# Kernel tuning notes

Measured on AMD Instinct MI355X. Metric: run time of the kernel, lower is better.

The kernel has to match this reference:

```python
import jax, jax.numpy as jnp
import numpy as np

NUM_SEGMENTS = 64
HIDDEN = 1024
RANK = 16
N = 8192


def _xavier(key, shape):
    fan_in, fan_out = shape[-2], shape[-1]
    limit = (6.0 / (fan_in + fan_out)) ** 0.5
    return jax.random.uniform(key, shape, jnp.float32, -limit, limit)


def setup_inputs() -> dict:
    key = jax.random.key(0)
    k1, k2, k3, k4 = jax.random.split(key, 4)
    return {
        "math_hidden_states": jax.random.normal(k1, (N, HIDDEN), jnp.float32),
        "segment_ids": jax.random.randint(k2, (N,), 0, NUM_SEGMENTS, jnp.int64),
        "A_matrices": _xavier(k3, (NUM_SEGMENTS, HIDDEN, RANK)),
        "B_matrices": _xavier(k4, (NUM_SEGMENTS, RANK, HIDDEN)),
        "bias": jnp.zeros((NUM_SEGMENTS, HIDDEN), jnp.float32),
    }


def reference(math_hidden_states, segment_ids, A_matrices, B_matrices, bias):
    # gather per-token low-rank factors: A [N,H,R], B [N,R,H]
    gathered_A = A_matrices[segment_ids]
    gathered_B = B_matrices[segment_ids]
    # intermediate = B @ x  -> [N, R]
    intermediate = jnp.einsum('nrh,nh->nr', gathered_B, math_hidden_states)
    # transformed = A @ intermediate -> [N, H]
    transformed = jnp.einsum('nhr,nr->nh', gathered_A, intermediate)
    return transformed + bias[segment_ids]
```

## Files before the change

### kernel.cpp

```cpp
#include <hip/hip_runtime.h>

#define HID 1024
#define RANK 16
#define NSEG 64
#define NCHUNK 16
#define NXCD 8

__global__ __launch_bounds__(256) void lora_v5(
    const float* __restrict__ x,
    const int*   __restrict__ seg,
    const float* __restrict__ A,
    const float* __restrict__ B,
    const float* __restrict__ bias,
    float*       __restrict__ out,
    int N)
{
    const int work = (blockIdx.x & (NXCD - 1)) * ((NSEG * NCHUNK) / NXCD)
                   + (blockIdx.x >> 3);
    const int s = work >> 4;
    const int c = work & (NCHUNK - 1);
    const int tid  = threadIdx.x;
    const int lane = tid & 63;
    const int wave = tid >> 6;

    __shared__ int   list[512];
    __shared__ int   cnt;
    __shared__ float red[4][16][68];
    __shared__ float inter_lds[2][4][RANK];

    if (tid == 0) cnt = 0;

    const float4* A4 = (const float4*)(A + (size_t)s * HID * RANK);
    float4 av[4][4];
    #pragma unroll
    for (int jh = 0; jh < 4; ++jh)
        #pragma unroll
        for (int q = 0; q < 4; ++q)
            av[jh][q] = A4[(size_t)(tid * 4 + jh) * (RANK / 4) + q];
    const float4 bia = ((const float4*)(bias + (size_t)s * HID))[tid];

    __syncthreads();

    const int chunkN = (N + NCHUNK - 1) / NCHUNK;
    const int i0 = c * chunkN;
    const int i1 = min(N, i0 + chunkN);
    for (int i = i0 + tid; i < i1; i += 256)
        if (seg[i] == s) list[atomicAdd(&cnt, 1)] = i;
    __syncthreads();
    const int m = cnt;
    if (m == 0) return;

    const float4* B4 = (const float4*)(B + (size_t)s * RANK * HID);
    const int v = lane & 15;
    const int q = lane >> 4;

    for (int t = 0; t < m; t += 4) {
        const int nt = min(4, m - t);
        int n[4];
        #pragma unroll
        for (int j = 0; j < 4; ++j)
            n[j] = list[t + (j < nt ? j : nt - 1)];

        float4 xv[4][4];
        #pragma unroll
        for (int j = 0; j < 4; ++j) {
            const float4* xr = (const float4*)(x + (size_t)n[j] * HID);
            #pragma unroll
            for (int k = 0; k < 4; ++k) xv[j][k] = xr[k * 64 + lane];
        }

        float acc[4][4];
        #pragma unroll
        for (int rr = 0; rr < 4; ++rr)
            #pragma unroll
            for (int j = 0; j < 4; ++j) acc[rr][j] = 0.f;

        #pragma unroll
        for (int rr = 0; rr < 4; ++rr) {
            const float4* Br = B4 + (size_t)(wave * 4 + rr) * (HID / 4);
            #pragma unroll
            for (int k = 0; k < 4; ++k) {
                float4 b = Br[k * 64 + lane];
                #pragma unroll
                for (int j = 0; j < 4; ++j)
                    acc[rr][j] += b.x * xv[j][k].x + b.y * xv[j][k].y
                                + b.z * xv[j][k].z + b.w * xv[j][k].w;
            }
        }

        #pragma unroll
        for (int rr = 0; rr < 4; ++rr)
            #pragma unroll
            for (int j = 0; j < 4; ++j)
                red[wave][rr * 4 + j][lane] = acc[rr][j];

        const float4* rp = (const float4*)&red[wave][v][q * 16];
        float4 r0 = rp[0], r1 = rp[1], r2 = rp[2], r3 = rp[3];
        float sum = ((r0.x + r0.y) + (r0.z + r0.w))
                  + ((r1.x + r1.y) + (r1.z + r1.w))
                  + ((r2.x + r2.y) + (r2.z + r2.w))
                  + ((r3.x + r3.y) + (r3.z + r3.w));
        sum += __shfl_xor(sum, 16, 64);
        sum += __shfl_xor(sum, 32, 64);

        const int buf = (t >> 2) & 1;
        if (lane < 16)
            inter_lds[buf][v & 3][wave * 4 + (v >> 2)] = sum;
        __syncthreads();

        #pragma unroll
        for (int j = 0; j < 4; ++j) {
            const float4* I4 = (const float4*)inter_lds[buf][j];
            float4 iv[4];
            #pragma unroll
            for (int qq = 0; qq < 4; ++qq) iv[qq] = I4[qq];
            float4 o = bia;
            float* op = (float*)&o;
            #pragma unroll
            for (int jh = 0; jh < 4; ++jh) {
                float a = 0.f;
                #pragma unroll
                for (int qq = 0; qq < 4; ++qq)
                    a += av[jh][qq].x * iv[qq].x + av[jh][qq].y * iv[qq].y
                       + av[jh][qq].z * iv[qq].z + av[jh][qq].w * iv[qq].w;
                op[jh] += a;
            }
            if (j < nt)
                ((float4*)(out + (size_t)n[j] * HID))[tid] = o;
        }
    }
}

extern "C" void kernel_launch(void* const* d_in, const int* in_sizes, int n_in,
                              void* d_out, int out_size, void* d_ws, size_t ws_size,
                              hipStream_t stream) {
    const float* x    = (const float*)d_in[0];
    const int*   seg  = (const int*)d_in[1];
    const float* A    = (const float*)d_in[2];
    const float* B    = (const float*)d_in[3];
    const float* bias = (const float*)d_in[4];
    float* out = (float*)d_out;

    const int n_tokens = in_sizes[1];

    lora_v5<<<NSEG * NCHUNK, 256, 0, stream>>>(x, seg, A, B, bias, out, n_tokens);
}
```

Measured before the change: 114.7 us.

## Replace per-chunk segment scanning with histogram-sort and one-tile-per-block apply

Adds a single-block histogram kernel and an atomic scatter kernel that bucket token indices by segment into a padded sorted list. The apply kernel then processes exactly one tile of four tokens per block. This removes the per-block scan of a whole chunk of segment ids (each id was read by all 64 segment blocks) and the serial inner loop over tokens. In exchange it adds two extra kernel launches, including a serial single-block histogram. It also reloads A and bias for every tile instead of reusing them across tokens.

```diff
diff --git a/kernel.cpp b/kernel.cpp
--- a/kernel.cpp
+++ b/kernel.cpp
@@ -3,32 +3,80 @@
 #define HID 1024
 #define RANK 16
 #define NSEG 64
-#define NCHUNK 16
 #define NXCD 8
 
-__global__ __launch_bounds__(256) void lora_v5(
+
+__global__ __launch_bounds__(1024) void k1_hist(
+    const int* __restrict__ seg, int N,
+    int* __restrict__ base_c, int* __restrict__ cursor,
+    int* __restrict__ sorted, int slots)
+{
+    __shared__ int hist[NSEG];
+    __shared__ int pbase[NSEG];
+    __shared__ int paddedTotal;
+    const int tid = threadIdx.x;
+    if (tid < NSEG) hist[tid] = 0;
+    __syncthreads();
+    for (int i = tid; i < N; i += 1024) atomicAdd(&hist[seg[i]], 1);
+    __syncthreads();
+    if (tid == 0) {
+        int run = 0;
+        for (int s = 0; s < NSEG; ++s) { pbase[s] = run; run += (hist[s] + 3) & ~3; }
+        paddedTotal = run;
+    }
+    __syncthreads();
+    if (tid < NSEG) {
+        base_c[tid] = pbase[tid];
+        cursor[tid] = 0;
+        const int c0 = hist[tid], c1 = (hist[tid] + 3) & ~3;
+        for (int k = c0; k < c1; ++k) sorted[pbase[tid] + k] = -1;
+    }
+    for (int i = paddedTotal + tid; i < slots; i += 1024) sorted[i] = -1;
+}
+
+__global__ __launch_bounds__(256) void k2_scatter(
+    const int* __restrict__ seg, int N,
+    const int* __restrict__ base_c, int* __restrict__ cursor,
+    int* __restrict__ sorted)
+{
+    const int i = blockIdx.x * 256 + threadIdx.x;
+    if (i < N) {
+        const int s = seg[i];
+        const int pos = atomicAdd(&cursor[s], 1);
+        sorted[base_c[s] + pos] = (s << 14) | i;
+    }
+}
+
+__global__ __launch_bounds__(256) void lora_apply(
     const float* __restrict__ x,
-    const int*   __restrict__ seg,
+    const int*   __restrict__ sorted,
     const float* __restrict__ A,
     const float* __restrict__ B,
     const float* __restrict__ bias,
     float*       __restrict__ out,
-    int N)
+    int tilesPerXcd)
 {
-    const int work = (blockIdx.x & (NXCD - 1)) * ((NSEG * NCHUNK) / NXCD)
-                   + (blockIdx.x >> 3);
-    const int s = work >> 4;
-    const int c = work & (NCHUNK - 1);
+    const int work = (blockIdx.x & (NXCD - 1)) * tilesPerXcd + (blockIdx.x >> 3);
     const int tid  = threadIdx.x;
     const int lane = tid & 63;
     const int wave = tid >> 6;
 
-    __shared__ int   list[512];
-    __shared__ int   cnt;
     __shared__ float red[4][16][68];
-    __shared__ float inter_lds[2][4][RANK];
+    __shared__ float inter_lds[4][RANK];
 
-    if (tid == 0) cnt = 0;
+    int e[4];
+    #pragma unroll
+    for (int j = 0; j < 4; ++j) e[j] = sorted[work * 4 + j];
+    if (e[0] < 0) return;
+    const int s = e[0] >> 14;
+
+    int  n[4];
+    bool valid[4];
+    #pragma unroll
+    for (int j = 0; j < 4; ++j) {
+        valid[j] = e[j] >= 0;
+        n[j] = (valid[j] ? e[j] : e[0]) & 16383;
+    }
 
     const float4* A4 = (const float4*)(A + (size_t)s * HID * RANK);
     float4 av[4][4];
@@ -39,95 +87,72 @@
             av[jh][q] = A4[(size_t)(tid * 4 + jh) * (RANK / 4) + q];
     const float4 bia = ((const float4*)(bias + (size_t)s * HID))[tid];
 
+    float4 xv[4][4];
+    #pragma unroll
+    for (int j = 0; j < 4; ++j) {
+        const float4* xr = (const float4*)(x + (size_t)n[j] * HID);
+        #pragma unroll
+        for (int k = 0; k < 4; ++k) xv[j][k] = xr[k * 64 + lane];
+    }
+
+    const float4* B4 = (const float4*)(B + (size_t)s * RANK * HID);
+    float acc[4][4];
+    #pragma unroll
+    for (int rr = 0; rr < 4; ++rr)
+        #pragma unroll
+        for (int j = 0; j < 4; ++j) acc[rr][j] = 0.f;
+
+    #pragma unroll
+    for (int rr = 0; rr < 4; ++rr) {
+        const float4* Br = B4 + (size_t)(wave * 4 + rr) * (HID / 4);
+        #pragma unroll
+        for (int k = 0; k < 4; ++k) {
+            float4 b = Br[k * 64 + lane];
+            #pragma unroll
+            for (int j = 0; j < 4; ++j)
+                acc[rr][j] += b.x * xv[j][k].x + b.y * xv[j][k].y
+                            + b.z * xv[j][k].z + b.w * xv[j][k].w;
+        }
+    }
+
+    #pragma unroll
+    for (int rr = 0; rr < 4; ++rr)
+        #pragma unroll
+        for (int j = 0; j < 4; ++j)
+            red[wave][rr * 4 + j][lane] = acc[rr][j];
+
+    const int v = lane & 15;
+    const int q = lane >> 4;
+    const float4* rp = (const float4*)&red[wave][v][q * 16];
+    float4 r0 = rp[0], r1 = rp[1], r2 = rp[2], r3 = rp[3];
+    float sum = ((r0.x + r0.y) + (r0.z + r0.w))
+              + ((r1.x + r1.y) + (r1.z + r1.w))
+              + ((r2.x + r2.y) + (r2.z + r2.w))
+              + ((r3.x + r3.y) + (r3.z + r3.w));
+    sum += __shfl_xor(sum, 16, 64);
+    sum += __shfl_xor(sum, 32, 64);
+    if (lane < 16) inter_lds[v & 3][wave * 4 + (v >> 2)] = sum;
     __syncthreads();
 
-    const int chunkN = (N + NCHUNK - 1) / NCHUNK;
-    const int i0 = c * chunkN;
-    const int i1 = min(N, i0 + chunkN);
-    for (int i = i0 + tid; i < i1; i += 256)
-        if (seg[i] == s) list[atomicAdd(&cnt, 1)] = i;
-    __syncthreads();
-    const int m = cnt;
-    if (m == 0) return;
-
-    const float4* B4 = (const float4*)(B + (size_t)s * RANK * HID);
-    const int v = lane & 15;
-    const int q = lane >> 4;
-
-    for (int t = 0; t < m; t += 4) {
-        const int nt = min(4, m - t);
-        int n[4];
+    #pragma unroll
+    for (int j = 0; j < 4; ++j) {
+        const float4* I4 = (const float4*)inter_lds[j];
+        float4 iv[4];
         #pragma unroll
-        for (int j = 0; j < 4; ++j)
-            n[j] = list[t + (j < nt ? j : nt - 1)];
-
-        float4 xv[4][4];
+        for (int qq = 0; qq < 4; ++qq) iv[qq] = I4[qq];
+        float4 o = bia;
+        float* op = (float*)&o;
         #pragma unroll
-        for (int j = 0; j < 4; ++j) {
-            const float4* xr = (const float4*)(x + (size_t)n[j] * HID);
+        for (int jh = 0; jh < 4; ++jh) {
+            float a = 0.f;
             #pragma unroll
-            for (int k = 0; k < 4; ++k) xv[j][k] = xr[k * 64 + lane];
+            for (int qq = 0; qq < 4; ++qq)
+                a += av[jh][qq].x * iv[qq].x + av[jh][qq].y * iv[qq].y
+                   + av[jh][qq].z * iv[qq].z + av[jh][qq].w * iv[qq].w;
+            op[jh] += a;
         }
-
-        float acc[4][4];
-        #pragma unroll
-        for (int rr = 0; rr < 4; ++rr)
-            #pragma unroll
-            for (int j = 0; j < 4; ++j) acc[rr][j] = 0.f;
-
-        #pragma unroll
-        for (int rr = 0; rr < 4; ++rr) {
-            const float4* Br = B4 + (size_t)(wave * 4 + rr) * (HID / 4);
-            #pragma unroll
-            for (int k = 0; k < 4; ++k) {
-                float4 b = Br[k * 64 + lane];
-                #pragma unroll
-                for (int j = 0; j < 4; ++j)
-                    acc[rr][j] += b.x * xv[j][k].x + b.y * xv[j][k].y
-                                + b.z * xv[j][k].z + b.w * xv[j][k].w;
-            }
-        }
-
-        #pragma unroll
-        for (int rr = 0; rr < 4; ++rr)
-            #pragma unroll
-            for (int j = 0; j < 4; ++j)
-                red[wave][rr * 4 + j][lane] = acc[rr][j];
-
-        const float4* rp = (const float4*)&red[wave][v][q * 16];
-        float4 r0 = rp[0], r1 = rp[1], r2 = rp[2], r3 = rp[3];
-        float sum = ((r0.x + r0.y) + (r0.z + r0.w))
-                  + ((r1.x + r1.y) + (r1.z + r1.w))
-                  + ((r2.x + r2.y) + (r2.z + r2.w))
-                  + ((r3.x + r3.y) + (r3.z + r3.w));
-        sum += __shfl_xor(sum, 16, 64);
-        sum += __shfl_xor(sum, 32, 64);
-
-        const int buf = (t >> 2) & 1;
-        if (lane < 16)
-            inter_lds[buf][v & 3][wave * 4 + (v >> 2)] = sum;
-        __syncthreads();
-
-        #pragma unroll
-        for (int j = 0; j < 4; ++j) {
-            const float4* I4 = (const float4*)inter_lds[buf][j];
-            float4 iv[4];
-            #pragma unroll
-            for (int qq = 0; qq < 4; ++qq) iv[qq] = I4[qq];
-            float4 o = bia;
-            float* op = (float*)&o;
-            #pragma unroll
-            for (int jh = 0; jh < 4; ++jh) {
-                float a = 0.f;
-                #pragma unroll
-                for (int qq = 0; qq < 4; ++qq)
-                    a += av[jh][qq].x * iv[qq].x + av[jh][qq].y * iv[qq].y
-                       + av[jh][qq].z * iv[qq].z + av[jh][qq].w * iv[qq].w;
-                op[jh] += a;
-            }
-            if (j < nt)
-                ((float4*)(out + (size_t)n[j] * HID))[tid] = o;
-        }
+        if (valid[j])
+            ((float4*)(out + (size_t)n[j] * HID))[tid] = o;
     }
 }
 
@@ -141,7 +166,17 @@
     const float* bias = (const float*)d_in[4];
     float* out = (float*)d_out;
 
-    const int n_tokens = in_sizes[1];
+    const int N = in_sizes[1];
 
-    lora_v5<<<NSEG * NCHUNK, 256, 0, stream>>>(x, seg, A, B, bias, out, n_tokens);
+    int tiles = ((N + 3) / 4 + NSEG + 7) & ~7;
+    const int slots = tiles * 4;
+
+    int* wsi    = (int*)d_ws;
+    int* base_c = wsi;
+    int* cursor = wsi + NSEG;
+    int* sorted = wsi + 2 * NSEG;
+
+    k1_hist   <<<1, 1024, 0, stream>>>(seg, N, base_c, cursor, sorted, slots);
+    k2_scatter<<<(N + 255) / 256, 256, 0, stream>>>(seg, N, base_c, cursor, sorted);
+    lora_apply<<<tiles, 256, 0, stream>>>(x, sorted, A, B, bias, out, tiles / NXCD);
 }
```

New measurement: 137.8 us. 20.2% more time.

## Keep B slice in registers and prefetch next token group's x rows

Applied to the files above, without the earlier changes.

Loads each wave's B rows into registers once before the token loop instead of re-reading them from global memory every iteration. Software-pipelines the x row loads so the next group of four tokens is fetched while the current group's dot products and reduction run. Adds a launch-bounds occupancy hint of 2 blocks. This raises register pressure (B, A and double x tiles in registers), which could cause spills or lower occupancy.

```diff
diff --git a/kernel.cpp b/kernel.cpp
--- a/kernel.cpp
+++ b/kernel.cpp
@@ -6,7 +6,7 @@
 #define NCHUNK 16
 #define NXCD 8
 
-__global__ __launch_bounds__(256) void lora_v5(
+__global__ __launch_bounds__(256, 2) void lora_v11(
     const float* __restrict__ x,
     const int*   __restrict__ seg,
     const float* __restrict__ A,
@@ -21,7 +21,7 @@
     const int c = work & (NCHUNK - 1);
     const int tid  = threadIdx.x;
     const int lane = tid & 63;
-    const int wave = tid >> 6;
+    const int w    = tid >> 6;
 
     __shared__ int   list[512];
     __shared__ int   cnt;
@@ -29,6 +29,14 @@
     __shared__ float inter_lds[2][4][RANK];
 
     if (tid == 0) cnt = 0;
+
+    const float4* B4 = (const float4*)(B + (size_t)s * RANK * HID);
+    float4 br[4][4];
+    #pragma unroll
+    for (int rr = 0; rr < 4; ++rr)
+        #pragma unroll
+        for (int k = 0; k < 4; ++k)
+            br[rr][k] = B4[(size_t)(w * 4 + rr) * (HID / 4) + k * 64 + lane];
 
     const float4* A4 = (const float4*)(A + (size_t)s * HID * RANK);
     float4 av[4][4];
@@ -50,41 +58,50 @@
     const int m = cnt;
     if (m == 0) return;
 
-    const float4* B4 = (const float4*)(B + (size_t)s * RANK * HID);
     const int v = lane & 15;
     const int q = lane >> 4;
 
+    int n[4];
+    #pragma unroll
+    for (int j = 0; j < 4; ++j) n[j] = list[min(j, m - 1)];
+    float4 xv[4][4];
+    #pragma unroll
+    for (int j = 0; j < 4; ++j) {
+        const float4* xr = (const float4*)(x + (size_t)n[j] * HID);
+        #pragma unroll
+        for (int k = 0; k < 4; ++k) xv[j][k] = xr[k * 64 + lane];
+    }
+
     for (int t = 0; t < m; t += 4) {
         const int nt = min(4, m - t);
-        int n[4];
+        int ns[4];
         #pragma unroll
-        for (int j = 0; j < 4; ++j)
-            n[j] = list[t + (j < nt ? j : nt - 1)];
-
-        float4 xv[4][4];
-        #pragma unroll
-        for (int j = 0; j < 4; ++j) {
-            const float4* xr = (const float4*)(x + (size_t)n[j] * HID);
-            #pragma unroll
-            for (int k = 0; k < 4; ++k) xv[j][k] = xr[k * 64 + lane];
-        }
+        for (int j = 0; j < 4; ++j) ns[j] = n[j];
 
         float acc[4][4];
         #pragma unroll
         for (int rr = 0; rr < 4; ++rr)
             #pragma unroll
             for (int j = 0; j < 4; ++j) acc[rr][j] = 0.f;
+        #pragma unroll
+        for (int k = 0; k < 4; ++k)
+            #pragma unroll
+            for (int j = 0; j < 4; ++j) {
+                const float4 xj = xv[j][k];
+                #pragma unroll
+                for (int rr = 0; rr < 4; ++rr)
+                    acc[rr][j] += br[rr][k].x * xj.x + br[rr][k].y * xj.y
+                                + br[rr][k].z * xj.z + br[rr][k].w * xj.w;
+            }
 
-        #pragma unroll
-        for (int rr = 0; rr < 4; ++rr) {
-            const float4* Br = B4 + (size_t)(wave * 4 + rr) * (HID / 4);
+        if (t + 4 < m) {
             #pragma unroll
-            for (int k = 0; k < 4; ++k) {
-                float4 b = Br[k * 64 + lane];
+            for (int j = 0; j < 4; ++j) n[j] = list[min(t + 4 + j, m - 1)];
+            #pragma unroll
+            for (int j = 0; j < 4; ++j) {
+                const float4* xr = (const float4*)(x + (size_t)n[j] * HID);
                 #pragma unroll
-                for (int j = 0; j < 4; ++j)
-                    acc[rr][j] += b.x * xv[j][k].x + b.y * xv[j][k].y
-                                + b.z * xv[j][k].z + b.w * xv[j][k].w;
+                for (int k = 0; k < 4; ++k) xv[j][k] = xr[k * 64 + lane];
             }
         }
 
@@ -92,9 +109,8 @@
         for (int rr = 0; rr < 4; ++rr)
             #pragma unroll
             for (int j = 0; j < 4; ++j)
-                red[wave][rr * 4 + j][lane] = acc[rr][j];
-
-        const float4* rp = (const float4*)&red[wave][v][q * 16];
+                red[w][rr * 4 + j][lane] = acc[rr][j];
+        const float4* rp = (const float4*)&red[w][v][q * 16];
         float4 r0 = rp[0], r1 = rp[1], r2 = rp[2], r3 = rp[3];
         float sum = ((r0.x + r0.y) + (r0.z + r0.w))
                   + ((r1.x + r1.y) + (r1.z + r1.w))
@@ -102,10 +118,8 @@
                   + ((r3.x + r3.y) + (r3.z + r3.w));
         sum += __shfl_xor(sum, 16, 64);
         sum += __shfl_xor(sum, 32, 64);
-
         const int buf = (t >> 2) & 1;
-        if (lane < 16)
-            inter_lds[buf][v & 3][wave * 4 + (v >> 2)] = sum;
+        if (lane < 16) inter_lds[buf][v & 3][w * 4 + (v >> 2)] = sum;
         __syncthreads();
 
         #pragma unroll
@@ -126,7 +140,7 @@
                 op[jh] += a;
             }
             if (j < nt)
-                ((float4*)(out + (size_t)n[j] * HID))[tid] = o;
+                ((float4*)(out + (size_t)ns[j] * HID))[tid] = o;
         }
     }
 }
@@ -143,5 +157,5 @@
 
     const int n_tokens = in_sizes[1];
 
-    lora_v5<<<NSEG * NCHUNK, 256, 0, stream>>>(x, seg, A, B, bias, out, n_tokens);
+    lora_v11<<<NSEG * NCHUNK, 256, 0, stream>>>(x, seg, A, B, bias, out, n_tokens);
 }
```

After: 147.9 us. 28.9% more time.
